# Kernel tuning notes

Hardware: AMD Instinct MI355X
Metric: run time of the kernel (lower is better)

## Reference

```python
import jax, jax.numpy as jnp
import numpy as np

EDGE_WIDTH = 128
NUM_HEADS = 8
DOT_DIM = EDGE_WIDTH // NUM_HEADS  # 16
B, N = 2, 256


def _layernorm(x, g, b, eps=1e-5):
    mu = jnp.mean(x, axis=-1, keepdims=True)
    var = jnp.var(x, axis=-1, keepdims=True)
    return (x - mu) * jax.lax.rsqrt(var + eps) * g + b


def setup_inputs() -> dict:
    key = jax.random.key(0)
    ks = jax.random.split(key, 8)
    W = EDGE_WIDTH
    H = NUM_HEADS
    s = lambda fan_in: 1.0 / np.sqrt(fan_in)
    return {
        "e": jax.random.normal(ks[0], (B, N, N, W), dtype=jnp.float32),
        "mask": jnp.zeros((B, N, N, 1), dtype=jnp.float32),
        "ln_g": jnp.ones((W,), dtype=jnp.float32),
        "ln_b": jnp.zeros((W,), dtype=jnp.float32),
        "W_V": jax.random.uniform(ks[1], (W, 2 * W), jnp.float32, -s(W), s(W)),
        "b_V": jnp.zeros((2 * W,), dtype=jnp.float32),
        "W_E": jax.random.uniform(ks[2], (W, 2 * H), jnp.float32, -s(W), s(W)),
        "b_E": jnp.zeros((2 * H,), dtype=jnp.float32),
        "W_O": jax.random.uniform(ks[3], (2 * W, W), jnp.float32, -s(2 * W), s(2 * W)),
        "b_O": jnp.zeros((W,), dtype=jnp.float32),
    }


def reference(e, mask, ln_g, ln_b, W_V, b_V, W_E, b_E, W_O, b_O):
    bsize, num_edges, _, embed_dim = e.shape
    H, D = NUM_HEADS, DOT_DIM

    e_ln = _layernorm(e, ln_g, ln_b)

    V = e_ln @ W_V + b_V                       # [B,N,N,2W]
    V_in, V_out = jnp.split(V, 2, axis=-1)     # each [B,N,N,W]
    V_in = V_in.reshape(bsize, num_edges, num_edges, D, H)
    V_out = V_out.reshape(bsize, num_edges, num_edges, D, H)

    E = e_ln @ W_E + b_E                       # [B,N,N,2H]
    E_in, E_out = jnp.split(E, 2, axis=-1)     # each [B,N,N,H]

    # NOTE: original module computes a scale factor but never applies it.
    A_in = jax.nn.softmax(E_in + mask, axis=2)            # softmax over k
    Va_in = jnp.einsum('bikh,bjkdh->bijdh', A_in, V_in)

    A_out = jax.nn.softmax(E_out + mask, axis=1)          # softmax over k
    Va_out = jnp.einsum('bkih,bkjdh->bijdh', A_out, V_out)

    Va = jnp.concatenate([Va_in, Va_out], axis=-1)        # [B,N,N,D,2H]
    Va = Va.reshape(bsize, num_edges, num_edges, embed_dim * 2)
    return Va @ W_O + b_O
```

## Files before the change

kernel.cpp:

```cpp
#include <hip/hip_runtime.h>
#include <hip/hip_bf16.h>
#include <stdint.h>


typedef short short8 __attribute__((ext_vector_type(8)));
typedef short short4v __attribute__((ext_vector_type(4)));
typedef float floatx4 __attribute__((ext_vector_type(4)));

#define AS1(p) ((const __attribute__((address_space(1))) void*)(p))
#define AS3(p) ((__attribute__((address_space(3))) void*)(p))

__device__ inline short f2bf(float v) {
    uint32_t u = __builtin_bit_cast(uint32_t, v);
    u += 0x7FFFu + ((u >> 16) & 1u);
    return (short)(u >> 16);
}

__global__ __launch_bounds__(128) void k0_prep(const float* __restrict__ WV,
                                               const float* __restrict__ WE,
                                               const float* __restrict__ WO,
                                               const float* __restrict__ ln_g,
                                               const float* __restrict__ ln_b,
                                               short* __restrict__ Wcat2,
                                               short* __restrict__ WOt2,
                                               const float* __restrict__ bV,
                                               const float* __restrict__ bE,
                                               float* __restrict__ bcat) {
    int bx = blockIdx.x, t = threadIdx.x;
    if (bx < 288) {
        int v = bx / 144, n = bx % 144, k = t;
        float val = 0.f;
        if (n < 128) val = WV[k * 256 + v * 128 + n];
        else if (n < 136) val = WE[k * 16 + v * 8 + (n - 128)];
        Wcat2[(v * 144 + n) * 128 + k] = f2bf(val * ln_g[k]);
    } else if (bx < 320) {
        int cc = bx - 288;
        for (int j = 0; j < 8; ++j) {
            int c = cc * 8 + j;
            WOt2[(cc * 128 + t) * 8 + j] =
                f2bf(WO[((c & 15) * 16 + (c >> 4)) * 128 + t]);
        }
    } else {
        for (int it = 0; it < 3; ++it) {
            int idx = it * 128 + t;
            if (idx < 288) {
                int v = idx / 144, n = idx % 144;
                float val = 0.f, dot = 0.f;
                if (n < 128) {
                    val = bV[v * 128 + n];
                    for (int k = 0; k < 128; ++k)
                        dot += ln_b[k] * WV[k * 256 + v * 128 + n];
                } else if (n < 136) {
                    val = bE[v * 8 + (n - 128)];
                    for (int k = 0; k < 128; ++k)
                        dot += ln_b[k] * WE[k * 16 + v * 8 + (n - 128)];
                }
                bcat[idx] = val + dot;
            }
        }
    }
}

__global__ __launch_bounds__(256, 3) void k1_ln_proj(
    const float* __restrict__ e, const float* __restrict__ ln_g,
    const float* __restrict__ ln_b, const float* __restrict__ mask,
    const short* __restrict__ Wcat2, const float* __restrict__ bcat,
    short* __restrict__ VinT, short* __restrict__ VoutT,
    short* __restrict__ Ain, short* __restrict__ AoutT) {
    (void)ln_g; (void)ln_b;
    __shared__ short Wlds[144 * 128];
    __shared__ float maskb[256];
    __shared__ float redm[4][8];
    __shared__ float reds[4][8];

    const int tid = threadIdx.x;
    const int fix = blockIdx.x;
    const int b = blockIdx.y;
    const int v = blockIdx.z;
    const int estride = v ? 256 : 1;
    const size_t ebase = (size_t)b * 65536 + (size_t)fix * (v ? 1 : 256);
    const short* Wv = Wcat2 + v * 144 * 128;
    const float* bc = bcat + v * 144;
    short* Vdst = v ? VoutT : VinT;
    short* Adst = v ? AoutT : Ain;

    const int lane = tid & 63, w = tid >> 6;
    const int ln_ = lane & 15, quad = lane >> 4;

#pragma unroll
    for (int it = 0; it < 9; ++it) {
        int gid = it * 256 + tid;
        int r = gid >> 4, p = gid & 15;
        const short* src = Wv + (r * 16 + (p ^ (r & 15))) * 8;
        __builtin_amdgcn_global_load_lds(AS1(src), AS3(&Wlds[gid * 8]), 16, 0, 0);
    }

    maskb[tid] = mask[(size_t)b * 65536 + (v ? (size_t)tid * 256 + fix
                                             : (size_t)fix * 256 + tid)];

    short8 a_frag[4][4];
#pragma unroll
    for (int mt = 0; mt < 4; ++mt) {
        int row = w * 64 + mt * 16 + ln_;
        const float* ep = e + (ebase + (size_t)row * estride) * 128 + quad * 8;
        float4 c0[4], c1[4];
        float s = 0.f, s2 = 0.f;
#pragma unroll
        for (int kk = 0; kk < 4; ++kk) {
            c0[kk] = *(const float4*)(ep + kk * 32);
            c1[kk] = *(const float4*)(ep + kk * 32 + 4);
            s += c0[kk].x + c0[kk].y + c0[kk].z + c0[kk].w +
                 c1[kk].x + c1[kk].y + c1[kk].z + c1[kk].w;
            s2 += c0[kk].x * c0[kk].x + c0[kk].y * c0[kk].y +
                  c0[kk].z * c0[kk].z + c0[kk].w * c0[kk].w +
                  c1[kk].x * c1[kk].x + c1[kk].y * c1[kk].y +
                  c1[kk].z * c1[kk].z + c1[kk].w * c1[kk].w;
        }
        s += __shfl_xor(s, 16); s2 += __shfl_xor(s2, 16);
        s += __shfl_xor(s, 32); s2 += __shfl_xor(s2, 32);
        float mean = s * 0.0078125f;
        float var = s2 * 0.0078125f - mean * mean;
        float rs = rsqrtf(var + 1e-5f);
#pragma unroll
        for (int kk = 0; kk < 4; ++kk) {
            short8 o;
            o[0] = f2bf((c0[kk].x - mean) * rs);
            o[1] = f2bf((c0[kk].y - mean) * rs);
            o[2] = f2bf((c0[kk].z - mean) * rs);
            o[3] = f2bf((c0[kk].w - mean) * rs);
            o[4] = f2bf((c1[kk].x - mean) * rs);
            o[5] = f2bf((c1[kk].y - mean) * rs);
            o[6] = f2bf((c1[kk].z - mean) * rs);
            o[7] = f2bf((c1[kk].w - mean) * rs);
            a_frag[mt][kk] = o;
        }
    }
    __syncthreads();

    float vE[16];

#pragma unroll
    for (int chunk = 0; chunk < 2; ++chunk) {
#pragma unroll
        for (int half = 0; half < 2; ++half) {
            floatx4 acc[4][2] = {};
#pragma unroll
            for (int kk = 0; kk < 4; ++kk) {
                int ckb = kk * 4 + quad;
                short8 bq[2];
#pragma unroll
                for (int nl = 0; nl < 2; ++nl) {
                    int n = chunk * 64 + (half * 2 + nl) * 16 + ln_;
                    bq[nl] = *(const short8*)&Wlds[(n * 16 + (ckb ^ (n & 15))) * 8];
                }
#pragma unroll
                for (int mt = 0; mt < 4; ++mt)
#pragma unroll
                    for (int nl = 0; nl < 2; ++nl)
                        acc[mt][nl] = __builtin_amdgcn_mfma_f32_16x16x32_bf16(
                            a_frag[mt][kk], bq[nl], acc[mt][nl], 0, 0, 0);
            }
#pragma unroll
            for (int nl = 0; nl < 2; ++nl) {
                int ntl = half * 2 + nl;
                int c = chunk * 64 + ntl * 16 + ln_;
                float bias = bc[c];
                int d = c >> 3, hh = c & 7;
                size_t rowbase = (((size_t)(b * 8 + hh) * 256 + fix) * 16 + d) * 256;
#pragma unroll
                for (int mt = 0; mt < 4; ++mt) {
                    short4v o;
#pragma unroll
                    for (int r = 0; r < 4; ++r) o[r] = f2bf(acc[mt][nl][r] + bias);
                    *(short4v*)(Vdst + rowbase + w * 64 + mt * 16 + quad * 4) = o;
                }
            }
        }
    }

    {
        floatx4 accE[4] = {};
#pragma unroll
        for (int kk = 0; kk < 4; ++kk) {
            int ckb = kk * 4 + quad;
            int n = 128 + ln_;
            short8 bq = *(const short8*)&Wlds[(n * 16 + (ckb ^ (n & 15))) * 8];
#pragma unroll
            for (int mt = 0; mt < 4; ++mt)
                accE[mt] = __builtin_amdgcn_mfma_f32_16x16x32_bf16(
                    a_frag[mt][kk], bq, accE[mt], 0, 0, 0);
        }
        float bias = bc[128 + ln_];
#pragma unroll
        for (int mt = 0; mt < 4; ++mt)
#pragma unroll
            for (int r = 0; r < 4; ++r) {
                int k = w * 64 + mt * 16 + quad * 4 + r;
                vE[mt * 4 + r] = accE[mt][r] + bias + maskb[k];
            }
    }

    {
        float m = vE[0];
#pragma unroll
        for (int i = 1; i < 16; ++i) m = fmaxf(m, vE[i]);
        m = fmaxf(m, __shfl_xor(m, 16));
        m = fmaxf(m, __shfl_xor(m, 32));
        if (quad == 0 && ln_ < 8) redm[w][ln_] = m;
        __syncthreads();
        int hs = ln_ & 7;
        float bmax = fmaxf(fmaxf(redm[0][hs], redm[1][hs]),
                           fmaxf(redm[2][hs], redm[3][hs]));
        float p[16], s = 0.f;
#pragma unroll
        for (int i = 0; i < 16; ++i) { p[i] = __expf(vE[i] - bmax); s += p[i]; }
        s += __shfl_xor(s, 16);
        s += __shfl_xor(s, 32);
        if (quad == 0 && ln_ < 8) reds[w][ln_] = s;
        __syncthreads();
        float inv = 1.f / (reds[0][hs] + reds[1][hs] + reds[2][hs] + reds[3][hs]);
        if (ln_ < 8) {
            size_t rowbase = (size_t)(b * 8 + ln_) * 65536 + (size_t)fix * 256;
#pragma unroll
            for (int mt = 0; mt < 4; ++mt) {
                short4v o;
#pragma unroll
                for (int r = 0; r < 4; ++r) o[r] = f2bf(p[mt * 4 + r] * inv);
                *(short4v*)(Adst + rowbase + w * 64 + mt * 16 + quad * 4) = o;
            }
        }
    }
}

__global__ __launch_bounds__(256, 3) void k3_einsum(const short* __restrict__ Ain,
                                                    const short* __restrict__ AoutT,
                                                    const short* __restrict__ VinT,
                                                    const short* __restrict__ VoutT,
                                                    short* __restrict__ VaP2) {
    __shared__ short AB[17408];
    const int tid = threadIdx.x, lane = tid & 63, w = tid >> 6;
    const int i0 = blockIdx.x * 128;
    const int jd0 = blockIdx.y * 128;
    const int z = blockIdx.z;
    const int b = z >> 4, part = (z >> 3) & 1, h = z & 7;

    const short* Abase = (part ? AoutT : Ain) + ((size_t)(b * 8 + h)) * 65536 + (size_t)i0 * 256;
    const short* Bbase = (part ? VoutT : VinT) + ((size_t)(b * 8 + h)) * 1048576 + (size_t)jd0 * 256;

    const int ln_ = lane & 15, quad = lane >> 4;
    const int m0 = (w >> 1) * 64, n0 = (w & 1) * 64;
    floatx4 acc[4][4] = {};

    for (int kt = 0; kt < 4; ++kt) {
        if (kt) __syncthreads();
        for (int it = 0; it < 8; ++it) {
            int cid = w * 512 + it * 64 + lane;
            int isB = cid >> 10;
            int lc = cid & 1023;
            int r = lc >> 3;
            int ck = (lc & 7) ^ (r & 7);
            const short* g = (isB ? Bbase : Abase) + r * 256 + kt * 64 + ck * 8;
            __builtin_amdgcn_global_load_lds(AS1(g), AS3(&AB[cid * 8]), 16, 0, 0);
        }
        __syncthreads();

#pragma unroll
        for (int kk = 0; kk < 2; ++kk) {
            int ckb = kk * 4 + quad;
            short8 aq[4], bq[4];
#pragma unroll
            for (int t = 0; t < 4; ++t) {
                int r = m0 + t * 16 + ln_;
                aq[t] = *(const short8*)&AB[(r * 8 + (ckb ^ (r & 7))) * 8];
            }
#pragma unroll
            for (int t = 0; t < 4; ++t) {
                int r = n0 + t * 16 + ln_;
                bq[t] = *(const short8*)&AB[(1024 + r * 8 + (ckb ^ (r & 7))) * 8];
            }
#pragma unroll
            for (int mt = 0; mt < 4; ++mt)
#pragma unroll
                for (int nt = 0; nt < 4; ++nt)
                    acc[mt][nt] = __builtin_amdgcn_mfma_f32_16x16x32_bf16(aq[mt], bq[nt], acc[mt][nt], 0, 0, 0);
        }
    }

    __syncthreads();
#pragma unroll
    for (int mt = 0; mt < 4; ++mt)
#pragma unroll
        for (int nt = 0; nt < 4; ++nt)
#pragma unroll
            for (int r = 0; r < 4; ++r) {
                int il = m0 + mt * 16 + quad * 4 + r;
                int jd = n0 + nt * 16 + ln_;
                AB[il * 136 + jd] = f2bf(acc[mt][nt][r]);
            }
    __syncthreads();

    const int ph = part * 8 + h;
    const int j0 = jd0 >> 4;
#pragma unroll
    for (int pp = 0; pp < 4; ++pp) {
        int pid = pp * 256 + tid;
        int il = pid >> 3, jl = pid & 7;
        size_t m = ((size_t)b * 256 + i0 + il) * 256 + j0 + jl;
        short8 v0 = *(const short8*)&AB[il * 136 + jl * 16];
        short8 v1 = *(const short8*)&AB[il * 136 + jl * 16 + 8];
        short* dst = VaP2 + ((size_t)ph * 131072 + m) * 16;
        *(short8*)dst = v0;
        *(short8*)(dst + 8) = v1;
    }
}

__global__ __launch_bounds__(256, 3) void k4_proj(const short* __restrict__ VaP2,
                                                  const short* __restrict__ WOt2,
                                                  const float* __restrict__ bO,
                                                  float* __restrict__ out) {
    __shared__ short A_s[16384];
    const int tid = threadIdx.x, lane = tid & 63, w = tid >> 6;
    const size_t m0g = (size_t)blockIdx.x * 128;
    const int ln_ = lane & 15, quad = lane >> 4;
    const int m0 = w * 32;
    floatx4 acc[2][8] = {};

    for (int kt = 0; kt < 2; ++kt) {
        if (kt) __syncthreads();
        for (int it = 0; it < 8; ++it) {
            int cid = w * 512 + it * 64 + lane;
            int p = cid >> 8, rm = cid & 255, half = rm >> 7, m = rm & 127;
            const short* g = VaP2 + ((size_t)(kt * 8 + p) * 131072 + m0g + m) * 16 + half * 8;
            __builtin_amdgcn_global_load_lds(AS1(g), AS3(&A_s[cid * 8]), 16, 0, 0);
        }
        __syncthreads();

#pragma unroll
        for (int kk = 0; kk < 4; ++kk) {
            int ckb = kk * 4 + quad;
            int p = ckb >> 1, hf = ckb & 1;
            short8 aq[2], bq[8];
#pragma unroll
            for (int mt = 0; mt < 2; ++mt) {
                int m = m0 + mt * 16 + ln_;
                aq[mt] = *(const short8*)&A_s[p * 2048 + hf * 1024 + m * 8];
            }
#pragma unroll
            for (int nt = 0; nt < 8; ++nt) {
                int wr = nt * 16 + ln_;
                bq[nt] = *(const short8*)(WOt2 + ((kt * 16 + ckb) * 128 + wr) * 8);
            }
#pragma unroll
            for (int mt = 0; mt < 2; ++mt)
#pragma unroll
                for (int nt = 0; nt < 8; ++nt)
                    acc[mt][nt] = __builtin_amdgcn_mfma_f32_16x16x32_bf16(aq[mt], bq[nt], acc[mt][nt], 0, 0, 0);
        }
    }

    float bo[8];
#pragma unroll
    for (int nt = 0; nt < 8; ++nt) bo[nt] = bO[nt * 16 + ln_];

#pragma unroll
    for (int mt = 0; mt < 2; ++mt)
#pragma unroll
        for (int r = 0; r < 4; ++r) {
            size_t mb = m0g + m0 + mt * 16 + quad * 4 + r;
#pragma unroll
            for (int nt = 0; nt < 8; ++nt)
                out[mb * 128 + nt * 16 + ln_] = acc[mt][nt][r] + bo[nt];
        }
}

extern "C" void kernel_launch(void* const* d_in, const int* in_sizes, int n_in,
                              void* d_out, int out_size, void* d_ws, size_t ws_size,
                              hipStream_t stream) {
    (void)in_sizes; (void)n_in; (void)out_size; (void)ws_size;
    const float* e    = (const float*)d_in[0];
    const float* mask = (const float*)d_in[1];
    const float* ln_g = (const float*)d_in[2];
    const float* ln_b = (const float*)d_in[3];
    const float* W_V  = (const float*)d_in[4];
    const float* b_V  = (const float*)d_in[5];
    const float* W_E  = (const float*)d_in[6];
    const float* b_E  = (const float*)d_in[7];
    const float* W_O  = (const float*)d_in[8];
    const float* b_O  = (const float*)d_in[9];
    float* out = (float*)d_out;

    char* ws = (char*)d_ws;
    short* VinT  = (short*)(ws + 0);
    short* VoutT = (short*)(ws + 33554432);
    short* Ain   = (short*)(ws + 67108864);
    short* AoutT = (short*)(ws + 69206016);
    short* VaP2  = (short*)(ws + 71303168);
    short* Wcat2 = (short*)(ws + 138412032);
    short* WOt2  = (short*)(ws + 138485760);
    float* bcat  = (float*)(ws + 138551296);

    k0_prep<<<321, 128, 0, stream>>>(W_V, W_E, W_O, ln_g, ln_b, Wcat2, WOt2,
                                     b_V, b_E, bcat);
    k1_ln_proj<<<dim3(256, 2, 2), 256, 0, stream>>>(e, ln_g, ln_b, mask, Wcat2,
                                                    bcat, VinT, VoutT, Ain, AoutT);
    k3_einsum<<<dim3(2, 32, 32), 256, 0, stream>>>(Ain, AoutT, VinT, VoutT, VaP2);
    k4_proj<<<1024, 256, 0, stream>>>(VaP2, WOt2, b_O, out);
}
```

Before: 233.8 us.

## Parallelize bias prep, raise k1 occupancy bound, remap einsum grid for L2 reuse

The bias-folding part of the prep kernel now uses one block per output with a wave-shuffle reduction across k, where before a single block ran serial 128-iteration loops. The LN/projection kernel's launch bounds minimum-blocks hint goes from 3 to 4, which may force fewer registers per thread. The einsum kernel switches to a 1D grid with a swizzled block-index mapping so that blocks sharing the same A tile and head run close together. These are three separate tweaks aimed at a serial tail, occupancy and cache locality, and the new register cap risks spills.

```diff
diff --git a/kernel.cpp b/kernel.cpp
--- a/kernel.cpp
+++ b/kernel.cpp
@@ -41,27 +41,29 @@
                 f2bf(WO[((c & 15) * 16 + (c >> 4)) * 128 + t]);
         }
     } else {
-        for (int it = 0; it < 3; ++it) {
-            int idx = it * 128 + t;
-            if (idx < 288) {
-                int v = idx / 144, n = idx % 144;
-                float val = 0.f, dot = 0.f;
-                if (n < 128) {
-                    val = bV[v * 128 + n];
-                    for (int k = 0; k < 128; ++k)
-                        dot += ln_b[k] * WV[k * 256 + v * 128 + n];
-                } else if (n < 136) {
-                    val = bE[v * 8 + (n - 128)];
-                    for (int k = 0; k < 128; ++k)
-                        dot += ln_b[k] * WE[k * 16 + v * 8 + (n - 128)];
-                }
-                bcat[idx] = val + dot;
-            }
-        }
-    }
-}
-
-__global__ __launch_bounds__(256, 3) void k1_ln_proj(
+        int idx = bx - 320;
+        int v = idx / 144, n = idx % 144;
+        int k = t;
+        float base = 0.f, wk = 0.f;
+        if (n < 128) {
+            base = bV[v * 128 + n];
+            wk = WV[k * 256 + v * 128 + n];
+        } else if (n < 136) {
+            base = bE[v * 8 + (n - 128)];
+            wk = WE[k * 16 + v * 8 + (n - 128)];
+        }
+        float p = ln_b[k] * wk;
+        p += __shfl_xor(p, 1);  p += __shfl_xor(p, 2);
+        p += __shfl_xor(p, 4);  p += __shfl_xor(p, 8);
+        p += __shfl_xor(p, 16); p += __shfl_xor(p, 32);
+        __shared__ float partial[2];
+        if ((t & 63) == 0) partial[t >> 6] = p;
+        __syncthreads();
+        if (t == 0) bcat[idx] = base + partial[0] + partial[1];
+    }
+}
+
+__global__ __launch_bounds__(256, 4) void k1_ln_proj(
     const float* __restrict__ e, const float* __restrict__ ln_g,
     const float* __restrict__ ln_b, const float* __restrict__ mask,
     const short* __restrict__ Wcat2, const float* __restrict__ bcat,
@@ -239,9 +241,13 @@
                                                     short* __restrict__ VaP2) {
     __shared__ short AB[17408];
     const int tid = threadIdx.x, lane = tid & 63, w = tid >> 6;
-    const int i0 = blockIdx.x * 128;
-    const int jd0 = blockIdx.y * 128;
-    const int z = blockIdx.z;
+
+    const int gid = blockIdx.x;
+    const int i0b = (gid >> 3) & 1;
+    const int q = (gid & 7) | ((gid >> 4) << 3);
+    const int i0 = i0b * 128;
+    const int jd0 = (q & 31) * 128;
+    const int z = q >> 5;
     const int b = z >> 4, part = (z >> 3) & 1, h = z & 7;
 
     const short* Abase = (part ? AoutT : Ain) + ((size_t)(b * 8 + h)) * 65536 + (size_t)i0 * 256;
@@ -399,10 +405,10 @@
     short* WOt2  = (short*)(ws + 138485760);
     float* bcat  = (float*)(ws + 138551296);
 
-    k0_prep<<<321, 128, 0, stream>>>(W_V, W_E, W_O, ln_g, ln_b, Wcat2, WOt2,
+    k0_prep<<<608, 128, 0, stream>>>(W_V, W_E, W_O, ln_g, ln_b, Wcat2, WOt2,
                                      b_V, b_E, bcat);
     k1_ln_proj<<<dim3(256, 2, 2), 256, 0, stream>>>(e, ln_g, ln_b, mask, Wcat2,
                                                     bcat, VinT, VoutT, Ain, AoutT);
-    k3_einsum<<<dim3(2, 32, 32), 256, 0, stream>>>(Ain, AoutT, VinT, VoutT, VaP2);
+    k3_einsum<<<2048, 256, 0, stream>>>(Ain, AoutT, VinT, VoutT, VaP2);
     k4_proj<<<1024, 256, 0, stream>>>(VaP2, WOt2, b_O, out);
 }
```

Result: slower. 257.2 us (+10.0%).
